# Optimization experiments

Hardware: AMD Instinct MI355X
Metric: run time of the kernel (lower is better)

The kernel has to match this reference:

```python
import jax, jax.numpy as jnp
import numpy as np

BN_EPS = 1e-5
INTERP_EPS = 1e-8


def _bn_relu(x, g, b, m, v):
    # eval-mode BatchNorm1d over channel dim (last axis here) + ReLU
    return jax.nn.relu((x - m) * (g / jnp.sqrt(v + BN_EPS)) + b)


def setup_inputs() -> dict:
    key = jax.random.key(0)
    ks = jax.random.split(key, 12)
    B, N, S, C1, C2 = 4, 16384, 1024, 128, 256
    Cin = C1 + C2  # 384
    H1, H2 = 256, 128
    inp = {
        "xyz1": jax.random.normal(ks[0], (B, N, 3), jnp.float32),
        "xyz2": jax.random.normal(ks[1], (B, S, 3), jnp.float32),
        "points1": jax.random.normal(ks[2], (B, N, C1), jnp.float32),
        "points2": jax.random.normal(ks[3], (B, S, C2), jnp.float32),
        # Conv1d(k=1, bias=False) weights: (out_ch, in_ch)
        "w1": jax.random.normal(ks[4], (H1, Cin), jnp.float32) * (1.0 / np.sqrt(Cin)),
        "g1": jax.random.uniform(ks[5], (H1,), jnp.float32, 0.5, 1.5),
        "b1": jax.random.normal(ks[6], (H1,), jnp.float32) * 0.1,
        "m1": jax.random.normal(ks[7], (H1,), jnp.float32) * 0.1,
        "v1": jax.random.uniform(ks[8], (H1,), jnp.float32, 0.5, 1.5),
        "w2": jax.random.normal(ks[9], (H2, H1), jnp.float32) * (1.0 / np.sqrt(H1)),
        "g2": jax.random.uniform(ks[10], (H2,), jnp.float32, 0.5, 1.5),
        "b2": jax.random.normal(ks[11], (H2,), jnp.float32) * 0.1,
        "m2": jnp.zeros((H2,), jnp.float32),
        "v2": jnp.ones((H2,), jnp.float32),
    }
    return inp


def reference(xyz1, xyz2, points1, points2, w1, g1, b1, m1, v1, w2, g2, b2, m2, v2):
    B, N, _ = xyz1.shape
    S = xyz2.shape[1]
    # squared pairwise distances (B, N, S) via ||a||^2 + ||b||^2 - 2 a.b
    sq = (
        jnp.sum(xyz1 * xyz1, -1)[:, :, None]
        + jnp.sum(xyz2 * xyz2, -1)[:, None, :]
        - 2.0 * jnp.einsum("bnd,bsd->bns", xyz1, xyz2)
    )
    neg_d, idx = jax.lax.top_k(-sq, 3)  # 3 nearest neighbors
    dists = -neg_d  # (B, N, 3) squared distances, ascending
    recip = 1.0 / (dists + INTERP_EPS)
    weight = recip / jnp.sum(recip, -1, keepdims=True)  # (B, N, 3)
    # gather neighbor features: (B, N, 3, C2)
    gathered = points2[jnp.arange(B)[:, None, None], idx]
    interpolated = jnp.einsum("bnk,bnkc->bnc", weight, gathered)
    new_points = jnp.concatenate([points1, interpolated], axis=-1)  # (B, N, Cin)
    h = _bn_relu(jnp.einsum("bnc,dc->bnd", new_points, w1), g1, b1, m1, v1)
    out = _bn_relu(jnp.einsum("bnc,dc->bnd", h, w2), g2, b2, m2, v2)
    return out
```

## Files before the change

kernel.cpp:

```cpp
#include <hip/hip_runtime.h>
#include <math.h>

#define B_    4
#define N_    16384
#define S_    1024
#define C1_   128
#define C2_   256
#define CIN_  384
#define H1_   256
#define H2_   128
#define BN_EPS_     1e-5f
#define INTERP_EPS_ 1e-8f

typedef _Float16 f16;
typedef _Float16 f16x4 __attribute__((ext_vector_type(4)));
typedef _Float16 f16x8 __attribute__((ext_vector_type(8)));
typedef float    f32x4 __attribute__((ext_vector_type(4)));

#define GLD16(g, l) \
  __builtin_amdgcn_global_load_lds((const __attribute__((address_space(1))) void*)(g), \
                                   (__attribute__((address_space(3))) void*)(l), 16, 0, 0)

#define WS_IDX 0
#define WS_W   786432
#define WS_H   1572864
#define WS_W1F 35127296
#define WS_W2F 35323904
#define WS_SC1 35389440
#define WS_SH1 35390464
#define WS_SC2 35391488
#define WS_SH2 35392000

__global__ __launch_bounds__(256) void prep_kernel(
    const float* __restrict__ w1, const float* __restrict__ w2,
    const float* __restrict__ g1, const float* __restrict__ b1,
    const float* __restrict__ m1, const float* __restrict__ v1,
    const float* __restrict__ g2, const float* __restrict__ b2,
    const float* __restrict__ m2, const float* __restrict__ v2,
    f16* __restrict__ w1f, f16* __restrict__ w2f,
    float* __restrict__ sc1, float* __restrict__ sh1,
    float* __restrict__ sc2, float* __restrict__ sh2)
{
    const int t = blockIdx.x * 256 + threadIdx.x;
    if (t < 98304) {
        w1f[t] = (f16)w1[t];
    } else if (t < 131072) {
        w2f[t - 98304] = (f16)w2[t - 98304];
    } else if (t < 131328) {
        const int c = t - 131072;
        const float s = g1[c] / sqrtf(v1[c] + BN_EPS_);
        sc1[c] = s; sh1[c] = b1[c] - m1[c] * s;
    } else if (t < 131456) {
        const int c = t - 131328;
        const float s = g2[c] / sqrtf(v2[c] + BN_EPS_);
        sc2[c] = s; sh2[c] = b2[c] - m2[c] * s;
    }
}

#define INSERT4(e, ei) do { \
    if ((e) < d[3]) { \
      if ((e) < d[2]) { d[3] = d[2]; id[3] = id[2]; \
        if ((e) < d[1]) { d[2] = d[1]; id[2] = id[1]; \
          if ((e) < d[0]) { d[1] = d[0]; id[1] = id[0]; d[0] = (e); id[0] = (ei); } \
          else { d[1] = (e); id[1] = (ei); } } \
        else { d[2] = (e); id[2] = (ei); } } \
      else { d[3] = (e); id[3] = (ei); } } } while (0)
#define CSWAP(a_, b_) do { \
    if (rd[b_] < rd[a_] || (rd[b_] == rd[a_] && ri[b_] < ri[a_])) { \
      double td = rd[a_]; rd[a_] = rd[b_]; rd[b_] = td; \
      int ti = ri[a_]; ri[a_] = ri[b_]; ri[b_] = ti; } } while (0)

__global__ __launch_bounds__(256) void topk_kernel(
    const float* __restrict__ xyz1, const float* __restrict__ xyz2,
    int* __restrict__ idx_out, float* __restrict__ w_out)
{
    __shared__ float4 q[S_ + 8];
    const int b     = blockIdx.x >> 9;
    const int pbase = (blockIdx.x & 511) << 5;
    const int t     = threadIdx.x;

    for (int i = t; i < S_; i += 256) {
        const float* s = &xyz2[((size_t)b * S_ + i) * 3];
        float4 v; v.x = s[0]; v.y = s[1]; v.z = s[2]; v.w = 0.0f;
        q[i + (i >> 7)] = v;
    }
    __syncthreads();

    const int p     = pbase + (t >> 3);
    const int chunk = t & 7;
    const int qb    = chunk * 129;
    const float* pp = &xyz1[((size_t)b * N_ + p) * 3];
    const float px = pp[0], py = pp[1], pz = pp[2];

    float d[4] = {1e30f, 1e30f, 1e30f, 1e30f};
    int  id[4] = {0, 0, 0, 0};

    for (int i = 0; i < 128; i += 4) {
        float dd[4];
        #pragma unroll
        for (int u = 0; u < 4; ++u) {
            const float4 c = q[qb + i + u];
            const float dx = px - c.x, dy = py - c.y, dz = pz - c.z;
            dd[u] = fmaf(dx, dx, fmaf(dy, dy, dz * dz));
        }
        const float m4 = fminf(fminf(dd[0], dd[1]), fminf(dd[2], dd[3]));
        if (__ballot(m4 < d[3])) {
            #pragma unroll
            for (int u = 0; u < 4; ++u) {
                const float e = dd[u];
                const int  ei = (chunk << 7) + i + u;
                INSERT4(e, ei);
            }
        }
    }

    #pragma unroll
    for (int msk = 1; msk <= 4; msk <<= 1) {
        float e0 = __shfl_xor(d[0], msk), e1 = __shfl_xor(d[1], msk);
        float e2 = __shfl_xor(d[2], msk), e3 = __shfl_xor(d[3], msk);
        int   j0 = __shfl_xor(id[0], msk), j1 = __shfl_xor(id[1], msk);
        int   j2 = __shfl_xor(id[2], msk), j3 = __shfl_xor(id[3], msk);
        INSERT4(e0, j0); INSERT4(e1, j1); INSERT4(e2, j2); INSERT4(e3, j3);
    }

    if (chunk == 0) {
        const double px6 = px, py6 = py, pz6 = pz;
        double rd[4]; int ri[4];
        #pragma unroll
        for (int j = 0; j < 4; ++j) {
            const int s = id[j]; ri[j] = s;
            const float4 c = q[s + (s >> 7)];
            const double dx = px6 - (double)c.x, dy = py6 - (double)c.y, dz = pz6 - (double)c.z;
            rd[j] = dx * dx + dy * dy + dz * dz;
        }
        CSWAP(0, 1); CSWAP(2, 3); CSWAP(0, 2); CSWAP(1, 3); CSWAP(1, 2);
        const float r0 = 1.0f / ((float)rd[0] + INTERP_EPS_);
        const float r1 = 1.0f / ((float)rd[1] + INTERP_EPS_);
        const float r2 = 1.0f / ((float)rd[2] + INTERP_EPS_);
        const float rs = r0 + r1 + r2;
        const int base = (b * N_ + p) * 3;
        idx_out[base] = ri[0]; idx_out[base + 1] = ri[1]; idx_out[base + 2] = ri[2];
        w_out[base] = r0 / rs; w_out[base + 1] = r1 / rs; w_out[base + 2] = r2 / rs;
    }
}

__device__ __forceinline__ void mfma_step1(const f16* As, const f16* Bs,
                                           f32x4 (&acc)[4][8],
                                           int wr, int wc, int lrow, int lhi)
{
    f16x8 af[4], bf[8];
    #pragma unroll
    for (int m = 0; m < 4; ++m)
        af[m] = *(const f16x8*)&As[(wr * 64 + m * 16 + lrow) * 32 + lhi * 8];
    #pragma unroll
    for (int n = 0; n < 8; ++n)
        bf[n] = *(const f16x8*)&Bs[(wc * 128 + n * 16 + lrow) * 32 + lhi * 8];
    #pragma unroll
    for (int m = 0; m < 4; ++m)
        #pragma unroll
        for (int n = 0; n < 8; ++n)
            acc[m][n] = __builtin_amdgcn_mfma_f32_16x16x32_f16(af[m], bf[n], acc[m][n], 0, 0, 0);
}

__global__ __launch_bounds__(256, 2) void gemm1_kernel(
    const float* __restrict__ points1, const float* __restrict__ points2,
    const int* __restrict__ idx, const float* __restrict__ wts,
    const f16* __restrict__ w1f,
    const float* __restrict__ sc1v, const float* __restrict__ sh1v,
    f16* __restrict__ h)
{
    __shared__ __align__(16) f16 As[128 * 32];
    __shared__ __align__(16) f16 Bs[256 * 32];

    const int t = threadIdx.x;
    const int w = t >> 6;
    const int lane = t & 63;
    const int wr = w >> 1, wc = w & 1;
    const int lrow = lane & 15, lhi = lane >> 4;
    const int rowbase = blockIdx.x * 128;

    const int srow = t >> 1, khalf = t & 1;
    const int R = rowbase + srow;
    const int bb = R >> 14;
    const int mb = R * 3;
    const int i0 = idx[mb], i1 = idx[mb + 1], i2 = idx[mb + 2];
    const float w0 = wts[mb], w1w = wts[mb + 1], w2w = wts[mb + 2];
    const float* p2b = points2 + (size_t)bb * S_ * C2_;
    const float* p1r = points1 + (size_t)R * C1_;
    f16* asrow = &As[srow * 32 + khalf * 16];

    f32x4 acc[4][8] = {};

    for (int kb = 0; kb < C1_; kb += 32) {
        __syncthreads();
        const float* src = p1r + kb + khalf * 16;
        #pragma unroll
        for (int g4 = 0; g4 < 4; ++g4) {
            const float4 v = *(const float4*)(src + g4 * 4);
            f16x4 o = {(f16)v.x, (f16)v.y, (f16)v.z, (f16)v.w};
            *(f16x4*)(asrow + g4 * 4) = o;
        }
        #pragma unroll
        for (int j = 0; j < 4; ++j) {
            const int c = j * 256 + t;
            GLD16(w1f + (size_t)(c >> 2) * CIN_ + kb + (c & 3) * 8,
                  (char*)Bs + (j * 4096 + w * 1024));
        }
        __syncthreads();
        mfma_step1(As, Bs, acc, wr, wc, lrow, lhi);
    }

    for (int kb = C1_; kb < CIN_; kb += 32) {
        __syncthreads();
        const int c0 = (kb - C1_) + khalf * 16;
        #pragma unroll
        for (int g4 = 0; g4 < 4; ++g4) {
            const int c = c0 + g4 * 4;
            const float4 f0 = *(const float4*)&p2b[(size_t)i0 * C2_ + c];
            const float4 f1 = *(const float4*)&p2b[(size_t)i1 * C2_ + c];
            const float4 f2 = *(const float4*)&p2b[(size_t)i2 * C2_ + c];
            const float x = fmaf(w0, f0.x, fmaf(w1w, f1.x, w2w * f2.x));
            const float y = fmaf(w0, f0.y, fmaf(w1w, f1.y, w2w * f2.y));
            const float z = fmaf(w0, f0.z, fmaf(w1w, f1.z, w2w * f2.z));
            const float u = fmaf(w0, f0.w, fmaf(w1w, f1.w, w2w * f2.w));
            f16x4 o = {(f16)x, (f16)y, (f16)z, (f16)u};
            *(f16x4*)(asrow + g4 * 4) = o;
        }
        #pragma unroll
        for (int j = 0; j < 4; ++j) {
            const int c = j * 256 + t;
            GLD16(w1f + (size_t)(c >> 2) * CIN_ + kb + (c & 3) * 8,
                  (char*)Bs + (j * 4096 + w * 1024));
        }
        __syncthreads();
        mfma_step1(As, Bs, acc, wr, wc, lrow, lhi);
    }

    #pragma unroll
    for (int n = 0; n < 8; ++n) {
        const int col = wc * 128 + n * 16 + lrow;
        const float sc = sc1v[col], sh = sh1v[col];
        #pragma unroll
        for (int m = 0; m < 4; ++m) {
            const int row0 = rowbase + wr * 64 + m * 16 + lhi * 4;
            #pragma unroll
            for (int i = 0; i < 4; ++i) {
                const float v = fmaxf(fmaf(acc[m][n][i], sc, sh), 0.0f);
                h[(size_t)(row0 + i) * H1_ + col] = (f16)v;
            }
        }
    }
}

__global__ __launch_bounds__(256, 2) void gemm2_kernel(
    const f16* __restrict__ hin, const f16* __restrict__ w2f,
    const float* __restrict__ sc2v, const float* __restrict__ sh2v,
    float* __restrict__ out)
{
    __shared__ __align__(16) f16 As[128 * 32];
    __shared__ __align__(16) f16 Bs[128 * 32];

    const int t = threadIdx.x;
    const int w = t >> 6;
    const int lane = t & 63;
    const int wr = w >> 1, wc = w & 1;
    const int lrow = lane & 15, lhi = lane >> 4;
    const int rowbase = blockIdx.x * 128;

    f32x4 acc[4][4] = {};

    for (int kb = 0; kb < H1_; kb += 32) {
        __syncthreads();
        #pragma unroll
        for (int j = 0; j < 2; ++j) {
            const int c = j * 256 + t;
            GLD16(hin + (size_t)(rowbase + (c >> 2)) * H1_ + kb + (c & 3) * 8,
                  (char*)As + (j * 4096 + w * 1024));
            GLD16(w2f + (size_t)(c >> 2) * H1_ + kb + (c & 3) * 8,
                  (char*)Bs + (j * 4096 + w * 1024));
        }
        __syncthreads();
        f16x8 af[4], bf[4];
        #pragma unroll
        for (int m = 0; m < 4; ++m)
            af[m] = *(const f16x8*)&As[(wr * 64 + m * 16 + lrow) * 32 + lhi * 8];
        #pragma unroll
        for (int n = 0; n < 4; ++n)
            bf[n] = *(const f16x8*)&Bs[(wc * 64 + n * 16 + lrow) * 32 + lhi * 8];
        #pragma unroll
        for (int m = 0; m < 4; ++m)
            #pragma unroll
            for (int n = 0; n < 4; ++n)
                acc[m][n] = __builtin_amdgcn_mfma_f32_16x16x32_f16(af[m], bf[n], acc[m][n], 0, 0, 0);
    }

    #pragma unroll
    for (int n = 0; n < 4; ++n) {
        const int col = wc * 64 + n * 16 + lrow;
        const float sc = sc2v[col], sh = sh2v[col];
        #pragma unroll
        for (int m = 0; m < 4; ++m) {
            const int row0 = rowbase + wr * 64 + m * 16 + lhi * 4;
            #pragma unroll
            for (int i = 0; i < 4; ++i) {
                out[(size_t)(row0 + i) * H2_ + col] = fmaxf(fmaf(acc[m][n][i], sc, sh), 0.0f);
            }
        }
    }
}

extern "C" void kernel_launch(void* const* d_in, const int* in_sizes, int n_in,
                              void* d_out, int out_size, void* d_ws, size_t ws_size,
                              hipStream_t stream) {
    const float* xyz1    = (const float*)d_in[0];
    const float* xyz2    = (const float*)d_in[1];
    const float* points1 = (const float*)d_in[2];
    const float* points2 = (const float*)d_in[3];
    const float* w1      = (const float*)d_in[4];
    const float* g1      = (const float*)d_in[5];
    const float* b1      = (const float*)d_in[6];
    const float* m1      = (const float*)d_in[7];
    const float* v1      = (const float*)d_in[8];
    const float* w2      = (const float*)d_in[9];
    const float* g2      = (const float*)d_in[10];
    const float* b2      = (const float*)d_in[11];
    const float* m2      = (const float*)d_in[12];
    const float* v2      = (const float*)d_in[13];
    float* out = (float*)d_out;

    char* ws = (char*)d_ws;
    int*   idx_ws = (int*)(ws + WS_IDX);
    float* w_ws   = (float*)(ws + WS_W);
    f16*   h_ws   = (f16*)(ws + WS_H);
    f16*   w1f    = (f16*)(ws + WS_W1F);
    f16*   w2f    = (f16*)(ws + WS_W2F);
    float* sc1    = (float*)(ws + WS_SC1);
    float* sh1    = (float*)(ws + WS_SH1);
    float* sc2    = (float*)(ws + WS_SC2);
    float* sh2    = (float*)(ws + WS_SH2);

    topk_kernel<<<dim3(B_ * (N_ / 32)), dim3(256), 0, stream>>>(xyz1, xyz2, idx_ws, w_ws);
    prep_kernel<<<dim3(514), dim3(256), 0, stream>>>(w1, w2, g1, b1, m1, v1,
                                                     g2, b2, m2, v2,
                                                     w1f, w2f, sc1, sh1, sc2, sh2);
    gemm1_kernel<<<dim3(512), dim3(256), 0, stream>>>(points1, points2, idx_ws, w_ws,
                                                      w1f, sc1, sh1, h_ws);
    gemm2_kernel<<<dim3(512), dim3(256), 0, stream>>>(h_ws, w2f, sc2, sh2, out);
}
```

Baseline: 204.2 us.

## Split interpolation into own kernel and use branchless packed-key top-k

The top-k search now packs a truncated float distance with the 10-bit index into one u32 key and keeps five candidates with a branchless min/max insertion network. The final order is fixed by recomputing exact double-precision distances and sorting the five. Neighbour indices are packed into one word per point. Feature interpolation moves out of gemm1 into a separate kernel that writes an f16 interpolated matrix, which gemm1 then streams into LDS with async global-to-LDS loads instead of doing scattered gathers inside its main loop. This adds an extra kernel launch and a 32MB intermediate write and read.

After: 185.9 us. 1.1x faster.

```diff
diff --git a/kernel.cpp b/kernel.cpp
--- a/kernel.cpp
+++ b/kernel.cpp
@@ -16,20 +16,22 @@
 typedef _Float16 f16x4 __attribute__((ext_vector_type(4)));
 typedef _Float16 f16x8 __attribute__((ext_vector_type(8)));
 typedef float    f32x4 __attribute__((ext_vector_type(4)));
+typedef unsigned int u32;
 
 #define GLD16(g, l) \
   __builtin_amdgcn_global_load_lds((const __attribute__((address_space(1))) void*)(g), \
                                    (__attribute__((address_space(3))) void*)(l), 16, 0, 0)
 
-#define WS_IDX 0
-#define WS_W   786432
-#define WS_H   1572864
-#define WS_W1F 35127296
-#define WS_W2F 35323904
-#define WS_SC1 35389440
-#define WS_SH1 35390464
-#define WS_SC2 35391488
-#define WS_SH2 35392000
+#define WS_IDXP 0
+#define WS_W    262144
+#define WS_XI   1048576
+#define WS_H    34603008
+#define WS_W1F  68157440
+#define WS_W2F  68354048
+#define WS_SC1  68419584
+#define WS_SH1  68420608
+#define WS_SC2  68421632
+#define WS_SH2  68422144
 
 __global__ __launch_bounds__(256) void prep_kernel(
     const float* __restrict__ w1, const float* __restrict__ w2,
@@ -57,14 +59,16 @@
     }
 }
 
-#define INSERT4(e, ei) do { \
-    if ((e) < d[3]) { \
-      if ((e) < d[2]) { d[3] = d[2]; id[3] = id[2]; \
-        if ((e) < d[1]) { d[2] = d[1]; id[2] = id[1]; \
-          if ((e) < d[0]) { d[1] = d[0]; id[1] = id[0]; d[0] = (e); id[0] = (ei); } \
-          else { d[1] = (e); id[1] = (ei); } } \
-        else { d[2] = (e); id[2] = (ei); } } \
-      else { d[3] = (e); id[3] = (ei); } } } while (0)
+__device__ __forceinline__ u32 umin_(u32 a, u32 b) { return a < b ? a : b; }
+__device__ __forceinline__ u32 umax_(u32 a, u32 b) { return a > b ? a : b; }
+
+#define KINS(k) do { \
+    u32 c1 = umax_(s0, (k)); s0 = umin_(s0, (k)); \
+    u32 c2 = umax_(s1, c1);  s1 = umin_(s1, c1);  \
+    u32 c3 = umax_(s2, c2);  s2 = umin_(s2, c2);  \
+    u32 c4 = umax_(s3, c3);  s3 = umin_(s3, c3);  \
+    s4 = umin_(s4, c4); } while (0)
+
 #define CSWAP(a_, b_) do { \
     if (rd[b_] < rd[a_] || (rd[b_] == rd[a_] && ri[b_] < ri[a_])) { \
       double td = rd[a_]; rd[a_] = rd[b_]; rd[b_] = td; \
@@ -72,7 +76,7 @@
 
 __global__ __launch_bounds__(256) void topk_kernel(
     const float* __restrict__ xyz1, const float* __restrict__ xyz2,
-    int* __restrict__ idx_out, float* __restrict__ w_out)
+    u32* __restrict__ idxp_out, float* __restrict__ w_out)
 {
     __shared__ float4 q[S_ + 8];
     const int b     = blockIdx.x >> 9;
@@ -89,59 +93,87 @@
     const int p     = pbase + (t >> 3);
     const int chunk = t & 7;
     const int qb    = chunk * 129;
+    const int ebase = chunk << 7;
     const float* pp = &xyz1[((size_t)b * N_ + p) * 3];
     const float px = pp[0], py = pp[1], pz = pp[2];
 
-    float d[4] = {1e30f, 1e30f, 1e30f, 1e30f};
-    int  id[4] = {0, 0, 0, 0};
+    u32 s0 = 0xFFFFFFFFu, s1 = 0xFFFFFFFFu, s2 = 0xFFFFFFFFu,
+        s3 = 0xFFFFFFFFu, s4 = 0xFFFFFFFFu;
 
     for (int i = 0; i < 128; i += 4) {
-        float dd[4];
         #pragma unroll
         for (int u = 0; u < 4; ++u) {
             const float4 c = q[qb + i + u];
             const float dx = px - c.x, dy = py - c.y, dz = pz - c.z;
-            dd[u] = fmaf(dx, dx, fmaf(dy, dy, dz * dz));
-        }
-        const float m4 = fminf(fminf(dd[0], dd[1]), fminf(dd[2], dd[3]));
-        if (__ballot(m4 < d[3])) {
-            #pragma unroll
-            for (int u = 0; u < 4; ++u) {
-                const float e = dd[u];
-                const int  ei = (chunk << 7) + i + u;
-                INSERT4(e, ei);
-            }
+            const float dd = fmaf(dx, dx, fmaf(dy, dy, dz * dz));
+            const u32 k = (__float_as_uint(dd) & 0xFFFFFC00u) | (u32)(ebase + i + u);
+            KINS(k);
         }
     }
 
     #pragma unroll
     for (int msk = 1; msk <= 4; msk <<= 1) {
-        float e0 = __shfl_xor(d[0], msk), e1 = __shfl_xor(d[1], msk);
-        float e2 = __shfl_xor(d[2], msk), e3 = __shfl_xor(d[3], msk);
-        int   j0 = __shfl_xor(id[0], msk), j1 = __shfl_xor(id[1], msk);
-        int   j2 = __shfl_xor(id[2], msk), j3 = __shfl_xor(id[3], msk);
-        INSERT4(e0, j0); INSERT4(e1, j1); INSERT4(e2, j2); INSERT4(e3, j3);
+        u32 e0 = __shfl_xor(s0, msk), e1 = __shfl_xor(s1, msk);
+        u32 e2 = __shfl_xor(s2, msk), e3 = __shfl_xor(s3, msk);
+        u32 e4 = __shfl_xor(s4, msk);
+        KINS(e0); KINS(e1); KINS(e2); KINS(e3); KINS(e4);
     }
 
     if (chunk == 0) {
         const double px6 = px, py6 = py, pz6 = pz;
-        double rd[4]; int ri[4];
-        #pragma unroll
-        for (int j = 0; j < 4; ++j) {
-            const int s = id[j]; ri[j] = s;
-            const float4 c = q[s + (s >> 7)];
+        double rd[5]; int ri[5];
+        const u32 ks[5] = {s0, s1, s2, s3, s4};
+        #pragma unroll
+        for (int j = 0; j < 5; ++j) {
+            const int si = (int)(ks[j] & 1023u); ri[j] = si;
+            const float4 c = q[si + (si >> 7)];
             const double dx = px6 - (double)c.x, dy = py6 - (double)c.y, dz = pz6 - (double)c.z;
             rd[j] = dx * dx + dy * dy + dz * dz;
         }
-        CSWAP(0, 1); CSWAP(2, 3); CSWAP(0, 2); CSWAP(1, 3); CSWAP(1, 2);
+        CSWAP(0,1); CSWAP(1,2); CSWAP(0,1); CSWAP(2,3); CSWAP(1,2);
+        CSWAP(0,1); CSWAP(3,4); CSWAP(2,3); CSWAP(1,2); CSWAP(0,1);
         const float r0 = 1.0f / ((float)rd[0] + INTERP_EPS_);
         const float r1 = 1.0f / ((float)rd[1] + INTERP_EPS_);
         const float r2 = 1.0f / ((float)rd[2] + INTERP_EPS_);
         const float rs = r0 + r1 + r2;
-        const int base = (b * N_ + p) * 3;
-        idx_out[base] = ri[0]; idx_out[base + 1] = ri[1]; idx_out[base + 2] = ri[2];
-        w_out[base] = r0 / rs; w_out[base + 1] = r1 / rs; w_out[base + 2] = r2 / rs;
-    }
+        const int row = b * N_ + p;
+        idxp_out[row] = (u32)ri[0] | ((u32)ri[1] << 10) | ((u32)ri[2] << 20);
+        w_out[row * 3 + 0] = r0 / rs;
+        w_out[row * 3 + 1] = r1 / rs;
+        w_out[row * 3 + 2] = r2 / rs;
+    }
+}
+
+__global__ __launch_bounds__(256) void interp_kernel(
+    const float* __restrict__ points2, const u32* __restrict__ idxp,
+    const float* __restrict__ wts, f16* __restrict__ xi)
+{
+    const int row  = blockIdx.x * 8 + (threadIdx.x >> 5);
+    const int lane = threadIdx.x & 31;
+    const int bb   = row >> 14;
+    const u32 u    = idxp[row];
+    const int i0 = (int)(u & 1023u), i1 = (int)((u >> 10) & 1023u), i2 = (int)(u >> 20);
+    const float w0 = wts[row * 3], w1w = wts[row * 3 + 1], w2w = wts[row * 3 + 2];
+    const float* p2b = points2 + (size_t)bb * S_ * C2_;
+    const int c0 = lane * 8;
+
+    const float4 a0 = *(const float4*)&p2b[i0 * C2_ + c0];
+    const float4 a1 = *(const float4*)&p2b[i0 * C2_ + c0 + 4];
+    const float4 b0 = *(const float4*)&p2b[i1 * C2_ + c0];
+    const float4 b1 = *(const float4*)&p2b[i1 * C2_ + c0 + 4];
+    const float4 d0 = *(const float4*)&p2b[i2 * C2_ + c0];
+    const float4 d1 = *(const float4*)&p2b[i2 * C2_ + c0 + 4];
+
+    f16x8 o;
+    o[0] = (f16)fmaf(w0, a0.x, fmaf(w1w, b0.x, w2w * d0.x));
+    o[1] = (f16)fmaf(w0, a0.y, fmaf(w1w, b0.y, w2w * d0.y));
+    o[2] = (f16)fmaf(w0, a0.z, fmaf(w1w, b0.z, w2w * d0.z));
+    o[3] = (f16)fmaf(w0, a0.w, fmaf(w1w, b0.w, w2w * d0.w));
+    o[4] = (f16)fmaf(w0, a1.x, fmaf(w1w, b1.x, w2w * d1.x));
+    o[5] = (f16)fmaf(w0, a1.y, fmaf(w1w, b1.y, w2w * d1.y));
+    o[6] = (f16)fmaf(w0, a1.z, fmaf(w1w, b1.z, w2w * d1.z));
+    o[7] = (f16)fmaf(w0, a1.w, fmaf(w1w, b1.w, w2w * d1.w));
+    *(f16x8*)&xi[(size_t)row * C2_ + c0] = o;
 }
 
 __device__ __forceinline__ void mfma_step1(const f16* As, const f16* Bs,
@@ -163,8 +195,7 @@
 }
 
 __global__ __launch_bounds__(256, 2) void gemm1_kernel(
-    const float* __restrict__ points1, const float* __restrict__ points2,
-    const int* __restrict__ idx, const float* __restrict__ wts,
+    const float* __restrict__ points1, const f16* __restrict__ xi,
     const f16* __restrict__ w1f,
     const float* __restrict__ sc1v, const float* __restrict__ sh1v,
     f16* __restrict__ h)
@@ -180,13 +211,7 @@
     const int rowbase = blockIdx.x * 128;
 
     const int srow = t >> 1, khalf = t & 1;
-    const int R = rowbase + srow;
-    const int bb = R >> 14;
-    const int mb = R * 3;
-    const int i0 = idx[mb], i1 = idx[mb + 1], i2 = idx[mb + 2];
-    const float w0 = wts[mb], w1w = wts[mb + 1], w2w = wts[mb + 2];
-    const float* p2b = points2 + (size_t)bb * S_ * C2_;
-    const float* p1r = points1 + (size_t)R * C1_;
+    const float* p1r = points1 + (size_t)(rowbase + srow) * C1_;
     f16* asrow = &As[srow * 32 + khalf * 16];
 
     f32x4 acc[4][8] = {};
@@ -212,19 +237,12 @@
 
     for (int kb = C1_; kb < CIN_; kb += 32) {
         __syncthreads();
-        const int c0 = (kb - C1_) + khalf * 16;
-        #pragma unroll
-        for (int g4 = 0; g4 < 4; ++g4) {
-            const int c = c0 + g4 * 4;
-            const float4 f0 = *(const float4*)&p2b[(size_t)i0 * C2_ + c];
-            const float4 f1 = *(const float4*)&p2b[(size_t)i1 * C2_ + c];
-            const float4 f2 = *(const float4*)&p2b[(size_t)i2 * C2_ + c];
-            const float x = fmaf(w0, f0.x, fmaf(w1w, f1.x, w2w * f2.x));
-            const float y = fmaf(w0, f0.y, fmaf(w1w, f1.y, w2w * f2.y));
-            const float z = fmaf(w0, f0.z, fmaf(w1w, f1.z, w2w * f2.z));
-            const float u = fmaf(w0, f0.w, fmaf(w1w, f1.w, w2w * f2.w));
-            f16x4 o = {(f16)x, (f16)y, (f16)z, (f16)u};
-            *(f16x4*)(asrow + g4 * 4) = o;
+        const int kk = kb - C1_;
+        #pragma unroll
+        for (int j = 0; j < 2; ++j) {
+            const int c = j * 256 + t;
+            GLD16(xi + (size_t)(rowbase + (c >> 2)) * C2_ + kk + (c & 3) * 8,
+                  (char*)As + (j * 4096 + w * 1024));
         }
         #pragma unroll
         for (int j = 0; j < 4; ++j) {
@@ -329,21 +347,22 @@
     float* out = (float*)d_out;
 
     char* ws = (char*)d_ws;
-    int*   idx_ws = (int*)(ws + WS_IDX);
-    float* w_ws   = (float*)(ws + WS_W);
-    f16*   h_ws   = (f16*)(ws + WS_H);
-    f16*   w1f    = (f16*)(ws + WS_W1F);
-    f16*   w2f    = (f16*)(ws + WS_W2F);
-    float* sc1    = (float*)(ws + WS_SC1);
-    float* sh1    = (float*)(ws + WS_SH1);
-    float* sc2    = (float*)(ws + WS_SC2);
-    float* sh2    = (float*)(ws + WS_SH2);
-
-    topk_kernel<<<dim3(B_ * (N_ / 32)), dim3(256), 0, stream>>>(xyz1, xyz2, idx_ws, w_ws);
+    u32*   idxp_ws = (u32*)(ws + WS_IDXP);
+    float* w_ws    = (float*)(ws + WS_W);
+    f16*   xi_ws   = (f16*)(ws + WS_XI);
+    f16*   h_ws    = (f16*)(ws + WS_H);
+    f16*   w1f     = (f16*)(ws + WS_W1F);
+    f16*   w2f     = (f16*)(ws + WS_W2F);
+    float* sc1     = (float*)(ws + WS_SC1);
+    float* sh1     = (float*)(ws + WS_SH1);
+    float* sc2     = (float*)(ws + WS_SC2);
+    float* sh2     = (float*)(ws + WS_SH2);
+
+    topk_kernel<<<dim3(B_ * (N_ / 32)), dim3(256), 0, stream>>>(xyz1, xyz2, idxp_ws, w_ws);
     prep_kernel<<<dim3(514), dim3(256), 0, stream>>>(w1, w2, g1, b1, m1, v1,
                                                      g2, b2, m2, v2,
                                                      w1f, w2f, sc1, sh1, sc2, sh2);
-    gemm1_kernel<<<dim3(512), dim3(256), 0, stream>>>(points1, points2, idx_ws, w_ws,
-                                                      w1f, sc1, sh1, h_ws);
+    interp_kernel<<<dim3(B_ * N_ / 8), dim3(256), 0, stream>>>(points2, idxp_ws, w_ws, xi_ws);
+    gemm1_kernel<<<dim3(512), dim3(256), 0, stream>>>(points1, xi_ws, w1f, sc1, sh1, h_ws);
     gemm2_kernel<<<dim3(512), dim3(256), 0, stream>>>(h_ws, w2f, sc2, sh2, out);
 }
```
